# Performance work log

Hardware: AMD Instinct MI355X
Metric: run time of the kernel (lower is better)

The kernel has to match this reference:

```python
import jax, jax.numpy as jnp
import numpy as np

GAMMA = 1.0  # gamma=1, train_gamma=False -> constant
K = 3        # kernel_size


def _l2norm(x, axis=-1):
    return x / jnp.sqrt(jnp.sum(x * x, axis=axis, keepdims=True))


def setup_inputs() -> dict:
    key = jax.random.key(0)
    ks = jax.random.split(key, 9)
    B_img, R, D = 48, 36, 1024
    B_cap, T = 48, 32
    Dq = D // 4  # reduce_proj = 4
    s = lambda fan: 1.0 / np.sqrt(fan)
    return {
        "img_embed": jax.random.normal(ks[0], (B_img, R, D), jnp.float32),
        "cap_embed": jax.random.normal(ks[1], (B_cap, T, D), jnp.float32),
        "lens": jax.random.randint(ks[2], (B_cap,), 1, T),
        "Wred": jax.random.normal(ks[3], (Dq, D), jnp.float32) * s(D),
        "bred": jax.random.normal(ks[4], (Dq,), jnp.float32) * s(D),
        "Wproj": jax.random.normal(ks[5], (D * K, Dq), jnp.float32) * s(Dq),
        "bproj": jax.random.normal(ks[6], (D * K,), jnp.float32) * s(Dq),
        "Wconv": jax.random.normal(ks[7], (D, D), jnp.float32) * s(D),
        "bconv": jax.random.normal(ks[8], (D,), jnp.float32) * s(D),
    }


def reference(img_embed, cap_embed, lens, Wred, bred, Wproj, bproj, Wconv, bconv):
    # img_embed: (B, R, D) -> x: (B, D, R);  cap_embed: (Q, T, D)
    B, R, D = img_embed.shape
    Q = cap_embed.shape[0]
    x = jnp.transpose(img_embed, (0, 2, 1))  # (B, D, R)

    # red_txt Conv1d(D, D/4, 1): only token 0 is used downstream
    cap0 = cap_embed[:, 0, :]                                 # (Q, D)
    cap_repr = cap0 @ Wred.T + bred                           # (Q, D/4)

    # dynamic depthwise kernel, softmax-normalized over the K taps
    wdyn = (cap_repr @ Wproj.T + bproj).reshape(Q, D, K)      # (Q, D, K)
    wdyn = jax.nn.softmax(wdyn, axis=-1)

    # depthwise conv (padding=1) applied to the FULL image batch per caption
    xpad = jnp.pad(x, ((0, 0), (0, 0), (1, 1)))
    shifts = jnp.stack([xpad[:, :, h:h + R] for h in range(K)], axis=-1)  # (B,D,R,K)
    conv_dyn = jnp.einsum('bcrk,qck->qbcr', shifts, wdyn)      # (Q, B, D, R)

    # pointwise Conv1d(D, D, 1)
    y = jnp.einsum('qbcr,dc->qbdr', conv_dyn, Wconv) + bconv[None, None, :, None]

    # softmax gate over regions, gated sum-pool, l2norm, cosine sim
    mask = jax.nn.softmax(y * GAMMA, axis=-1)
    img_vec = _l2norm(jnp.sum(mask * y, axis=-1), axis=-1)     # (Q, B, D)
    cap_vec = _l2norm(cap0, axis=-1)                           # (Q, D)
    sims = jnp.einsum('qbd,qd->bq', img_vec, cap_vec)          # (B_img, B_cap)
    return sims
```

## Files before the change

### kernel.cpp

```cpp
#include <hip/hip_runtime.h>

#define D_   1024
#define B_   48
#define Q_   48
#define R_   36
#define RP_  38
#define DQ_  256
#define NPQ_ 1728

typedef __attribute__((ext_vector_type(8))) short bf16x8;
typedef __attribute__((ext_vector_type(8))) unsigned short u16x8;
typedef __attribute__((ext_vector_type(4))) float f32x4;

static __device__ __forceinline__ unsigned short f2bf(float f) {
  union { float f; unsigned u; } v; v.f = f;
  unsigned r = v.u + 0x7fffu + ((v.u >> 16) & 1u);
  return (unsigned short)(r >> 16);
}
static __device__ __forceinline__ float bf2f(unsigned short h) {
  union { unsigned u; float f; } v; v.u = ((unsigned)h) << 16; return v.f;
}
static __device__ __forceinline__ void gload_lds16(const void* g, void* s) {
  __builtin_amdgcn_global_load_lds(
      (const __attribute__((address_space(1))) unsigned int*)g,
      (__attribute__((address_space(3))) unsigned int*)s, 16, 0, 0);
}

__global__ __launch_bounds__(256) void k_repr(const float* __restrict__ cap_embed,
    const float* __restrict__ Wred, const float* __restrict__ bred,
    float* __restrict__ repr)
{
  const int q = blockIdx.x;
  const int w = threadIdx.x >> 6, lane = threadIdx.x & 63;
  const int o = blockIdx.y * 4 + w;
  const float4* c4 = (const float4*)(cap_embed + (size_t)q * 32 * D_);
  const float4* wr = (const float4*)(Wred + (size_t)o * D_);
  float acc = 0.f;
  #pragma unroll
  for (int j = 0; j < 4; j++) {
    float4 a = wr[lane + j*64], c = c4[lane + j*64];
    acc += a.x*c.x + a.y*c.y + a.z*c.z + a.w*c.w;
  }
  #pragma unroll
  for (int off = 32; off > 0; off >>= 1) acc += __shfl_down(acc, off);
  if (lane == 0) repr[(size_t)q * DQ_ + o] = acc + bred[o];
}

__global__ __launch_bounds__(256) void k_wdyn(const float* __restrict__ repr,
    const float* __restrict__ Wproj, const float* __restrict__ bproj,
    float* __restrict__ wpl)
{
  const int q = blockIdx.x;
  const int w = threadIdx.x >> 6, lane = threadIdx.x & 63;
  const int d = blockIdx.y * 4 + w;
  float4 r4 = ((const float4*)(repr + (size_t)q * DQ_))[lane];
  float a0, a1, a2;
  {
    const float4* p0 = (const float4*)(Wproj + (size_t)(d*3 + 0) * DQ_);
    const float4* p1 = (const float4*)(Wproj + (size_t)(d*3 + 1) * DQ_);
    const float4* p2 = (const float4*)(Wproj + (size_t)(d*3 + 2) * DQ_);
    float4 v0 = p0[lane], v1 = p1[lane], v2 = p2[lane];
    a0 = v0.x*r4.x + v0.y*r4.y + v0.z*r4.z + v0.w*r4.w;
    a1 = v1.x*r4.x + v1.y*r4.y + v1.z*r4.z + v1.w*r4.w;
    a2 = v2.x*r4.x + v2.y*r4.y + v2.z*r4.z + v2.w*r4.w;
  }
  #pragma unroll
  for (int off = 32; off > 0; off >>= 1) {
    a0 += __shfl_down(a0, off);
    a1 += __shfl_down(a1, off);
    a2 += __shfl_down(a2, off);
  }
  if (lane == 0) {
    float l0 = a0 + bproj[d*3], l1 = a1 + bproj[d*3+1], l2 = a2 + bproj[d*3+2];
    float m = fmaxf(l0, fmaxf(l1, l2));
    float e0 = __expf(l0-m), e1 = __expf(l1-m), e2 = __expf(l2-m);
    float inv = 1.0f / (e0 + e1 + e2);
    wpl[((size_t)q*3 + 0) * D_ + d] = e0 * inv;
    wpl[((size_t)q*3 + 1) * D_ + d] = e1 * inv;
    wpl[((size_t)q*3 + 2) * D_ + d] = e2 * inv;
  }
}

__global__ __launch_bounds__(256) void k_xpad(const float* __restrict__ img,
                                              unsigned short* __restrict__ xpb)
{
  const int br = blockIdx.x;
  const int b = br / RP_, rp = br % RP_;
  const int c = threadIdx.x * 4;
  short4 o;
  if (rp == 0 || rp == RP_ - 1) { o.x = 0; o.y = 0; o.z = 0; o.w = 0; }
  else {
    float4 v = *(const float4*)&img[((size_t)b * R_ + (rp-1)) * D_ + c];
    o.x = (short)f2bf(v.x); o.y = (short)f2bf(v.y);
    o.z = (short)f2bf(v.z); o.w = (short)f2bf(v.w);
  }
  *(short4*)&xpb[(size_t)br * D_ + c] = o;
}

__global__ __launch_bounds__(256) void k_wcbf(const float* __restrict__ Wconv,
                                              unsigned short* __restrict__ wcbf)
{
  const int tid = blockIdx.x * 256 + threadIdx.x;
  const int m = tid >> 7;
  const int gg = tid & 127;
  const int tile = gg >> 2, g = gg & 3;
  const int gl = g ^ ((m >> 1) & 3);
  const float* src = Wconv + (size_t)m * D_ + tile * 32 + gl * 8;
  float4 v0 = *(const float4*)src, v1 = *(const float4*)(src + 4);
  u16x8 o;
  o[0] = f2bf(v0.x); o[1] = f2bf(v0.y); o[2] = f2bf(v0.z); o[3] = f2bf(v0.w);
  o[4] = f2bf(v1.x); o[5] = f2bf(v1.y); o[6] = f2bf(v1.z); o[7] = f2bf(v1.w);
  *(u16x8*)&wcbf[(size_t)m * D_ + tile * 32 + g * 8] = o;
}

__global__ __launch_bounds__(256) void k_cd(const unsigned short* __restrict__ xpb,
    const float* __restrict__ wpl, unsigned short* __restrict__ cd, int qstart)
{
  const int ql = blockIdx.y, qg = qstart + ql;
  const int t = threadIdx.x;
  const int bloc = t >> 7;
  const int b = blockIdx.x * 2 + bloc;
  const int gg = t & 127;
  const int tile = gg >> 2, g = gg & 3;
  const int ch = gg * 8;

  float w0[8], w1[8], w2[8];
  {
    const float4* p0 = (const float4*)(wpl + ((size_t)qg*3 + 0)*D_ + ch);
    const float4* p1 = (const float4*)(wpl + ((size_t)qg*3 + 1)*D_ + ch);
    const float4* p2 = (const float4*)(wpl + ((size_t)qg*3 + 2)*D_ + ch);
    float4 a0 = p0[0], a1 = p0[1], b0 = p1[0], b1 = p1[1], d0 = p2[0], d1 = p2[1];
    w0[0]=a0.x; w0[1]=a0.y; w0[2]=a0.z; w0[3]=a0.w; w0[4]=a1.x; w0[5]=a1.y; w0[6]=a1.z; w0[7]=a1.w;
    w1[0]=b0.x; w1[1]=b0.y; w1[2]=b0.z; w1[3]=b0.w; w1[4]=b1.x; w1[5]=b1.y; w1[6]=b1.z; w1[7]=b1.w;
    w2[0]=d0.x; w2[1]=d0.y; w2[2]=d0.z; w2[3]=d0.w; w2[4]=d1.x; w2[5]=d1.y; w2[6]=d1.z; w2[7]=d1.w;
  }
  const unsigned short* xb = xpb + (size_t)b * RP_ * D_ + ch;
  u16x8 ra = *(const u16x8*)&xb[0];
  u16x8 rb = *(const u16x8*)&xb[D_];
  unsigned short* outb = cd + ((size_t)ql * NPQ_ + (size_t)b * R_) * D_ + tile * 32;
  for (int r = 0; r < R_; r++) {
    u16x8 rc = *(const u16x8*)&xb[(size_t)(r + 2) * D_];
    u16x8 o;
    #pragma unroll
    for (int i = 0; i < 8; i++) {
      float y = w0[i]*bf2f(ra[i]) + w1[i]*bf2f(rb[i]) + w2[i]*bf2f(rc[i]);
      o[i] = f2bf(y);
    }
    int gp = g ^ (((b * 36 + r) >> 1) & 3);
    *(u16x8*)&outb[(size_t)r * D_ + gp * 8] = o;
    ra = rb; rb = rc;
  }
}

#define BM_ 256
#define BN_ 144
#define BK_ 64

__global__ __launch_bounds__(256, 2) void k_gemm(
    const unsigned short* __restrict__ wcbf, const unsigned short* __restrict__ cd,
    const float* __restrict__ bconv, float* __restrict__ imgvec, int qstart)
{
  __shared__ __align__(16) unsigned char smem[51200];
  unsigned short* As = (unsigned short*)smem;
  unsigned short* Bs = (unsigned short*)(smem + 32768);
  float* ep = (float*)smem;

  const int t = threadIdx.x;
  const int w = t >> 6, lane = t & 63;
  const int nt0 = blockIdx.x * BN_;
  const int dt0 = blockIdx.y * BM_;
  const int ql = blockIdx.z, qg = qstart + ql;

  f32x4 acc[4][9];
  #pragma unroll
  for (int mm = 0; mm < 4; mm++)
    #pragma unroll
    for (int nt = 0; nt < 9; nt++)
      acc[mm][nt] = (f32x4){0.f, 0.f, 0.f, 0.f};

  const int lrow = lane >> 2;
  const int lc8  = (lane & 3) * 8;
  const unsigned short* Ag = wcbf + (size_t)dt0 * D_ + lc8;
  const unsigned short* Bg = cd + ((size_t)ql * NPQ_ + nt0) * D_ + lc8;
  const int fr = lane & 15;
  const int fro = fr * 32 + ((((lane >> 4) ^ ((fr >> 1) & 3))) << 3);

  for (int k0 = 0; k0 < D_; k0 += BK_) {
    #pragma unroll
    for (int jj = 0; jj < 8; jj++) {
      int u = w + jj * 4;
      int ja = u >> 1, h = u & 1;
      gload_lds16(Ag + (size_t)(ja*16 + lrow) * D_ + k0 + h*32, As + u * 512);
    }
    for (int u = w; u < 18; u += 4) {
      int jb = u >> 1, h = u & 1;
      gload_lds16(Bg + (size_t)(jb*16 + lrow) * D_ + k0 + h*32, Bs + u * 512);
    }
    __syncthreads();
    #pragma unroll
    for (int s = 0; s < 2; s++) {
      bf16x8 aF[4], bF[9];
      #pragma unroll
      for (int mm = 0; mm < 4; mm++)
        aF[mm] = *(const bf16x8*)&As[((w*4 + mm)*2 + s) * 512 + fro];
      #pragma unroll
      for (int nt = 0; nt < 9; nt++)
        bF[nt] = *(const bf16x8*)&Bs[(nt*2 + s) * 512 + fro];
      #pragma unroll
      for (int mm = 0; mm < 4; mm++)
        #pragma unroll
        for (int nt = 0; nt < 9; nt++)
          acc[mm][nt] = __builtin_amdgcn_mfma_f32_16x16x32_bf16(aF[mm], bF[nt], acc[mm][nt], 0, 0, 0);
    }
    __syncthreads();
  }

  const int quad = lane >> 4;
  const int b0 = nt0 / R_;
  #pragma unroll
  for (int pp = 0; pp < 2; pp++) {
    #pragma unroll
    for (int p = 0; p < 2; p++) {
      if ((w >> 1) == pp) {
        #pragma unroll
        for (int mm = 0; mm < 4; mm++)
          #pragma unroll
          for (int nt = 0; nt < 9; nt++) {
            int col = nt * 16 + fr;
            int cl = col - 72 * p;
            if (cl >= 0 && cl < 72) {
              #pragma unroll
              for (int rg = 0; rg < 4; rg++) {
                int rloc = (w & 1) * 64 + mm * 16 + quad * 4 + rg;
                ep[rloc * 73 + cl] = acc[mm][nt][rg];
              }
            }
          }
      }
      __syncthreads();
      {
        int dloc = t >> 1, bloc = t & 1;
        int bg = b0 + p * 2 + bloc;
        int dg = dt0 + pp * 128 + dloc;
        const float* yr = ep + dloc * 73 + bloc * 36;
        float m = yr[0];
        for (int r = 1; r < R_; r++) m = fmaxf(m, yr[r]);
        float s = 0.f, wsum = 0.f;
        for (int r = 0; r < R_; r++) {
          float yv = yr[r];
          float e = __expf(yv - m);
          s += e; wsum += e * yv;
        }
        float img = wsum / s + bconv[dg];
        imgvec[((size_t)qg * B_ + bg) * D_ + dg] = img;
      }
      __syncthreads();
    }
  }
}

__global__ __launch_bounds__(256) void k_sims(const float* __restrict__ imgvec,
    const float* __restrict__ cap_embed, float* __restrict__ out)
{
  const int q = blockIdx.x, b = blockIdx.y, t = threadIdx.x;
  const float4* iv = (const float4*)(imgvec + ((size_t)q * B_ + b) * D_);
  const float4* cv = (const float4*)(cap_embed + (size_t)q * 32 * D_);
  float4 a = iv[t], c = cv[t];
  float ss = a.x*a.x + a.y*a.y + a.z*a.z + a.w*a.w;
  float sc = c.x*c.x + c.y*c.y + c.z*c.z + c.w*c.w;
  float dt = a.x*c.x + a.y*c.y + a.z*c.z + a.w*c.w;
  #pragma unroll
  for (int off = 32; off > 0; off >>= 1) {
    ss += __shfl_down(ss, off);
    sc += __shfl_down(sc, off);
    dt += __shfl_down(dt, off);
  }
  __shared__ float r1[4], r2[4], r3[4];
  if ((t & 63) == 0) { r1[t >> 6] = ss; r2[t >> 6] = sc; r3[t >> 6] = dt; }
  __syncthreads();
  if (t == 0) {
    ss = r1[0] + r1[1] + r1[2] + r1[3];
    sc = r2[0] + r2[1] + r2[2] + r2[3];
    dt = r3[0] + r3[1] + r3[2] + r3[3];
    out[(size_t)b * Q_ + q] = dt * rsqrtf(ss) * rsqrtf(sc);
  }
}

extern "C" void kernel_launch(void* const* d_in, const int* in_sizes, int n_in,
                              void* d_out, int out_size, void* d_ws, size_t ws_size,
                              hipStream_t stream)
{
  (void)in_sizes; (void)n_in; (void)out_size;
  const float* img   = (const float*)d_in[0];
  const float* cap   = (const float*)d_in[1];
  const float* Wred  = (const float*)d_in[3];
  const float* bred  = (const float*)d_in[4];
  const float* Wproj = (const float*)d_in[5];
  const float* bproj = (const float*)d_in[6];
  const float* Wconv = (const float*)d_in[7];
  const float* bconv = (const float*)d_in[8];
  float* out = (float*)d_out;

  char* ws = (char*)d_ws;
  const size_t XPB_B  = (size_t)B_ * RP_ * D_ * 2;
  const size_t WCBF_B = (size_t)D_ * D_ * 2;
  const size_t WPL_B  = (size_t)Q_ * 3 * D_ * 4;
  const size_t REPR_B = (size_t)Q_ * DQ_ * 4;
  const size_t IMGV_B = (size_t)Q_ * B_ * D_ * 4;
  unsigned short* xpb  = (unsigned short*)ws;
  unsigned short* wcbf = (unsigned short*)(ws + XPB_B);
  float* wpl    = (float*)(ws + XPB_B + WCBF_B);
  float* repr   = (float*)(ws + XPB_B + WCBF_B + WPL_B);
  float* imgvec = (float*)(ws + XPB_B + WCBF_B + WPL_B + REPR_B);
  const size_t FIXED = XPB_B + WCBF_B + WPL_B + REPR_B + IMGV_B;
  unsigned short* cdbuf = (unsigned short*)(ws + FIXED);
  const size_t PERQ = (size_t)NPQ_ * D_ * 2;

  int qchunk = 1;
  if (ws_size > FIXED + PERQ) {
    size_t c = (ws_size - FIXED) / PERQ;
    qchunk = (c > (size_t)Q_) ? Q_ : (int)c;
  }

  k_repr<<<dim3(Q_, 64), dim3(256), 0, stream>>>(cap, Wred, bred, repr);
  k_wdyn<<<dim3(Q_, 256), dim3(256), 0, stream>>>(repr, Wproj, bproj, wpl);
  k_xpad<<<dim3(B_ * RP_), dim3(256), 0, stream>>>(img, xpb);
  k_wcbf<<<dim3(512), dim3(256), 0, stream>>>(Wconv, wcbf);
  for (int q0 = 0; q0 < Q_; q0 += qchunk) {
    int qs = (Q_ - q0 < qchunk) ? (Q_ - q0) : qchunk;
    k_cd<<<dim3(B_ / 2, qs), dim3(256), 0, stream>>>(xpb, wpl, cdbuf, q0);
    k_gemm<<<dim3(NPQ_ / BN_, D_ / BM_, qs), dim3(256), 0, stream>>>(wcbf, cdbuf, bconv, imgvec, q0);
  }
  k_sims<<<dim3(Q_, B_), dim3(256), 0, stream>>>(imgvec, cap, out);
}
```

Measured before the change: 289.0 us.

## Merge preprocessing kernels and widen the GEMM epilogue to all 256 rows

The xpad, Wconv bf16 conversion and caption-reduction kernels are merged into one launch that branches on block index, cutting two kernel launches. The GEMM epilogue now stages all 256 output rows at once in a larger shared buffer (about 73 KB instead of 51 KB), so every thread runs the region softmax with fewer barrier rounds. The larger shared allocation may lower the number of GEMM blocks resident per CU below the two that launch_bounds requests.

```diff
diff --git a/kernel.cpp b/kernel.cpp
--- a/kernel.cpp
+++ b/kernel.cpp
@@ -26,24 +26,53 @@
       (__attribute__((address_space(3))) unsigned int*)s, 16, 0, 0);
 }
 
-__global__ __launch_bounds__(256) void k_repr(const float* __restrict__ cap_embed,
-    const float* __restrict__ Wred, const float* __restrict__ bred,
-    float* __restrict__ repr)
-{
-  const int q = blockIdx.x;
-  const int w = threadIdx.x >> 6, lane = threadIdx.x & 63;
-  const int o = blockIdx.y * 4 + w;
-  const float4* c4 = (const float4*)(cap_embed + (size_t)q * 32 * D_);
-  const float4* wr = (const float4*)(Wred + (size_t)o * D_);
-  float acc = 0.f;
-  #pragma unroll
-  for (int j = 0; j < 4; j++) {
-    float4 a = wr[lane + j*64], c = c4[lane + j*64];
-    acc += a.x*c.x + a.y*c.y + a.z*c.z + a.w*c.w;
-  }
-  #pragma unroll
-  for (int off = 32; off > 0; off >>= 1) acc += __shfl_down(acc, off);
-  if (lane == 0) repr[(size_t)q * DQ_ + o] = acc + bred[o];
+__global__ __launch_bounds__(256) void k_pre(
+    const float* __restrict__ img, unsigned short* __restrict__ xpb,
+    const float* __restrict__ Wconv, unsigned short* __restrict__ wcbf,
+    const float* __restrict__ cap_embed, const float* __restrict__ Wred,
+    const float* __restrict__ bred, float* __restrict__ repr)
+{
+  const int bx = blockIdx.x, t = threadIdx.x;
+  if (bx < B_ * RP_) {
+    const int b = bx / RP_, rp = bx % RP_;
+    const int c = t * 4;
+    short4 o;
+    if (rp == 0 || rp == RP_ - 1) { o.x = 0; o.y = 0; o.z = 0; o.w = 0; }
+    else {
+      float4 v = *(const float4*)&img[((size_t)b * R_ + (rp-1)) * D_ + c];
+      o.x = (short)f2bf(v.x); o.y = (short)f2bf(v.y);
+      o.z = (short)f2bf(v.z); o.w = (short)f2bf(v.w);
+    }
+    *(short4*)&xpb[(size_t)bx * D_ + c] = o;
+  } else if (bx < B_ * RP_ + 512) {
+    const int tid = (bx - B_ * RP_) * 256 + t;
+    const int m = tid >> 7;
+    const int gg = tid & 127;
+    const int tile = gg >> 2, g = gg & 3;
+    const int gl = g ^ ((m >> 1) & 3);
+    const float* src = Wconv + (size_t)m * D_ + tile * 32 + gl * 8;
+    float4 v0 = *(const float4*)src, v1 = *(const float4*)(src + 4);
+    u16x8 o;
+    o[0] = f2bf(v0.x); o[1] = f2bf(v0.y); o[2] = f2bf(v0.z); o[3] = f2bf(v0.w);
+    o[4] = f2bf(v1.x); o[5] = f2bf(v1.y); o[6] = f2bf(v1.z); o[7] = f2bf(v1.w);
+    *(u16x8*)&wcbf[(size_t)m * D_ + tile * 32 + g * 8] = o;
+  } else {
+    const int b2 = bx - (B_ * RP_ + 512);
+    const int q = b2 >> 6, yo = b2 & 63;
+    const int w = t >> 6, lane = t & 63;
+    const int o = yo * 4 + w;
+    const float4* c4 = (const float4*)(cap_embed + (size_t)q * 32 * D_);
+    const float4* wr = (const float4*)(Wred + (size_t)o * D_);
+    float acc = 0.f;
+    #pragma unroll
+    for (int j = 0; j < 4; j++) {
+      float4 a = wr[lane + j*64], c = c4[lane + j*64];
+      acc += a.x*c.x + a.y*c.y + a.z*c.z + a.w*c.w;
+    }
+    #pragma unroll
+    for (int off = 32; off > 0; off >>= 1) acc += __shfl_down(acc, off);
+    if (lane == 0) repr[(size_t)q * DQ_ + o] = acc + bred[o];
+  }
 }
 
 __global__ __launch_bounds__(256) void k_wdyn(const float* __restrict__ repr,
@@ -81,38 +110,6 @@
   }
 }
 
-__global__ __launch_bounds__(256) void k_xpad(const float* __restrict__ img,
-                                              unsigned short* __restrict__ xpb)
-{
-  const int br = blockIdx.x;
-  const int b = br / RP_, rp = br % RP_;
-  const int c = threadIdx.x * 4;
-  short4 o;
-  if (rp == 0 || rp == RP_ - 1) { o.x = 0; o.y = 0; o.z = 0; o.w = 0; }
-  else {
-    float4 v = *(const float4*)&img[((size_t)b * R_ + (rp-1)) * D_ + c];
-    o.x = (short)f2bf(v.x); o.y = (short)f2bf(v.y);
-    o.z = (short)f2bf(v.z); o.w = (short)f2bf(v.w);
-  }
-  *(short4*)&xpb[(size_t)br * D_ + c] = o;
-}
-
-__global__ __launch_bounds__(256) void k_wcbf(const float* __restrict__ Wconv,
-                                              unsigned short* __restrict__ wcbf)
-{
-  const int tid = blockIdx.x * 256 + threadIdx.x;
-  const int m = tid >> 7;
-  const int gg = tid & 127;
-  const int tile = gg >> 2, g = gg & 3;
-  const int gl = g ^ ((m >> 1) & 3);
-  const float* src = Wconv + (size_t)m * D_ + tile * 32 + gl * 8;
-  float4 v0 = *(const float4*)src, v1 = *(const float4*)(src + 4);
-  u16x8 o;
-  o[0] = f2bf(v0.x); o[1] = f2bf(v0.y); o[2] = f2bf(v0.z); o[3] = f2bf(v0.w);
-  o[4] = f2bf(v1.x); o[5] = f2bf(v1.y); o[6] = f2bf(v1.z); o[7] = f2bf(v1.w);
-  *(u16x8*)&wcbf[(size_t)m * D_ + tile * 32 + g * 8] = o;
-}
-
 __global__ __launch_bounds__(256) void k_cd(const unsigned short* __restrict__ xpb,
     const float* __restrict__ wpl, unsigned short* __restrict__ cd, int qstart)
 {
@@ -160,7 +157,7 @@
     const unsigned short* __restrict__ wcbf, const unsigned short* __restrict__ cd,
     const float* __restrict__ bconv, float* __restrict__ imgvec, int qstart)
 {
-  __shared__ __align__(16) unsigned char smem[51200];
+  __shared__ __align__(16) unsigned char smem[74752];
   unsigned short* As = (unsigned short*)smem;
   unsigned short* Bs = (unsigned short*)(smem + 32768);
   float* ep = (float*)smem;
@@ -218,44 +215,39 @@
   const int quad = lane >> 4;
   const int b0 = nt0 / R_;
   #pragma unroll
-  for (int pp = 0; pp < 2; pp++) {
-    #pragma unroll
-    for (int p = 0; p < 2; p++) {
-      if ((w >> 1) == pp) {
-        #pragma unroll
-        for (int mm = 0; mm < 4; mm++)
+  for (int p = 0; p < 2; p++) {
+    #pragma unroll
+    for (int mm = 0; mm < 4; mm++)
+      #pragma unroll
+      for (int nt = 0; nt < 9; nt++) {
+        int col = nt * 16 + fr;
+        int cl = col - 72 * p;
+        if (cl >= 0 && cl < 72) {
           #pragma unroll
-          for (int nt = 0; nt < 9; nt++) {
-            int col = nt * 16 + fr;
-            int cl = col - 72 * p;
-            if (cl >= 0 && cl < 72) {
-              #pragma unroll
-              for (int rg = 0; rg < 4; rg++) {
-                int rloc = (w & 1) * 64 + mm * 16 + quad * 4 + rg;
-                ep[rloc * 73 + cl] = acc[mm][nt][rg];
-              }
-            }
+          for (int rg = 0; rg < 4; rg++) {
+            int rloc = w * 64 + mm * 16 + quad * 4 + rg;
+            ep[rloc * 73 + cl] = acc[mm][nt][rg];
           }
+        }
       }
-      __syncthreads();
-      {
-        int dloc = t >> 1, bloc = t & 1;
-        int bg = b0 + p * 2 + bloc;
-        int dg = dt0 + pp * 128 + dloc;
-        const float* yr = ep + dloc * 73 + bloc * 36;
-        float m = yr[0];
-        for (int r = 1; r < R_; r++) m = fmaxf(m, yr[r]);
-        float s = 0.f, wsum = 0.f;
-        for (int r = 0; r < R_; r++) {
-          float yv = yr[r];
-          float e = __expf(yv - m);
-          s += e; wsum += e * yv;
-        }
-        float img = wsum / s + bconv[dg];
-        imgvec[((size_t)qg * B_ + bg) * D_ + dg] = img;
+    __syncthreads();
+    #pragma unroll
+    for (int bloc = 0; bloc < 2; bloc++) {
+      int bg = b0 + p * 2 + bloc;
+      int dg = dt0 + t;
+      const float* yr = ep + t * 73 + bloc * 36;
+      float m = yr[0];
+      for (int r = 1; r < R_; r++) m = fmaxf(m, yr[r]);
+      float s = 0.f, wsum = 0.f;
+      for (int r = 0; r < R_; r++) {
+        float yv = yr[r];
+        float e = __expf(yv - m);
+        s += e; wsum += e * yv;
       }
-      __syncthreads();
-    }
+      float img = wsum / s + bconv[dg];
+      imgvec[((size_t)qg * B_ + bg) * D_ + dg] = img;
+    }
+    __syncthreads();
   }
 }
 
@@ -322,10 +314,9 @@
     qchunk = (c > (size_t)Q_) ? Q_ : (int)c;
   }
 
-  k_repr<<<dim3(Q_, 64), dim3(256), 0, stream>>>(cap, Wred, bred, repr);
+  k_pre<<<dim3(B_ * RP_ + 512 + Q_ * 64), dim3(256), 0, stream>>>(
+      img, xpb, Wconv, wcbf, cap, Wred, bred, repr);
   k_wdyn<<<dim3(Q_, 256), dim3(256), 0, stream>>>(repr, Wproj, bproj, wpl);
-  k_xpad<<<dim3(B_ * RP_), dim3(256), 0, stream>>>(img, xpb);
-  k_wcbf<<<dim3(512), dim3(256), 0, stream>>>(Wconv, wcbf);
   for (int q0 = 0; q0 < Q_; q0 += qchunk) {
     int qs = (Q_ - q0 < qchunk) ? (Q_ - q0) : qchunk;
     k_cd<<<dim3(B_ / 2, qs), dim3(256), 0, stream>>>(xpb, wpl, cdbuf, q0);
```

Measured after the change: 287.6 us. About the same (-0.5%).
